# Kernel tuning notes

Measured on AMD Instinct MI355X. Metric: run time of the kernel, lower is better.

Reference implementation:

```python
import jax, jax.numpy as jnp
import numpy as np
from jax.ops import segment_sum, segment_max

N = 50000      # nodes
E_RAND = 800000
E = E_RAND + N  # random edges + self-loops
G = 4096       # graphs in batch
IN = 64        # input node feat dim
H = 4          # heads
F = 64         # per-head out feats
D = F          # gnn out feats (last agg = 'mean')
PH = 32        # predictor hidden (D // 2)
NEG_SLOPE = 0.2


def setup_inputs() -> dict:
    key = jax.random.key(0)
    ks = jax.random.split(key, 20)
    x = jax.random.normal(ks[0], (N, IN), dtype=jnp.float32)
    src = jnp.concatenate([jax.random.randint(ks[1], (E_RAND,), 0, N), jnp.arange(N)]).astype(jnp.int64)
    dst = jnp.concatenate([jax.random.randint(ks[2], (E_RAND,), 0, N), jnp.arange(N)]).astype(jnp.int64)
    gid = jnp.sort(jax.random.randint(ks[3], (N,), 0, G)).astype(jnp.int64)
    s = 0.1
    # layer 1: in=IN, flatten -> H*F
    W1 = jax.random.normal(ks[4], (IN, H * F), dtype=jnp.float32) * s
    al1 = jax.random.normal(ks[5], (H, F), dtype=jnp.float32) * s
    ar1 = jax.random.normal(ks[6], (H, F), dtype=jnp.float32) * s
    b1 = jnp.zeros((H * F,), dtype=jnp.float32)
    Wres1 = jax.random.normal(ks[7], (IN, H * F), dtype=jnp.float32) * s
    # layer 2: in=H*F, mean -> F
    W2 = jax.random.normal(ks[8], (H * F, H * F), dtype=jnp.float32) * s
    al2 = jax.random.normal(ks[9], (H, F), dtype=jnp.float32) * s
    ar2 = jax.random.normal(ks[10], (H, F), dtype=jnp.float32) * s
    b2 = jnp.zeros((H * F,), dtype=jnp.float32)
    Wres2 = jax.random.normal(ks[11], (H * F, H * F), dtype=jnp.float32) * s
    # WeightedSumAndMax atom-weighting
    Ww = jax.random.normal(ks[12], (D, 1), dtype=jnp.float32) * s
    bw = jnp.zeros((1,), dtype=jnp.float32)
    # predictor MLP: 2D -> PH -> 1
    Wp1 = jax.random.normal(ks[13], (2 * D, PH), dtype=jnp.float32) * s
    bp1 = jnp.zeros((PH,), dtype=jnp.float32)
    Wp2 = jax.random.normal(ks[14], (PH, 1), dtype=jnp.float32) * s
    bp2 = jnp.zeros((1,), dtype=jnp.float32)
    return dict(x=x, src=src, dst=dst, gid=gid,
                W1=W1, al1=al1, ar1=ar1, b1=b1, Wres1=Wres1,
                W2=W2, al2=al2, ar2=ar2, b2=b2, Wres2=Wres2,
                Ww=Ww, bw=bw, Wp1=Wp1, bp1=bp1, Wp2=Wp2, bp2=bp2)


def gat_conv(x, src, dst, W, al, ar, b, Wres, agg):
    n = x.shape[0]
    h, f = al.shape
    feat = (x @ W).reshape(n, h, f)                      # [N,H,F]
    el = jnp.einsum('nhf,hf->nh', feat, al)              # [N,H]
    er = jnp.einsum('nhf,hf->nh', feat, ar)
    e = jax.nn.leaky_relu(el[src] + er[dst], NEG_SLOPE)  # [E,H]
    # segment softmax over incoming edges per destination node
    m = segment_max(e, dst, num_segments=n)
    a = jnp.exp(e - m[dst])
    denom = segment_sum(a, dst, num_segments=n)
    attn = a / denom[dst]                                # [E,H]
    out = segment_sum(feat[src] * attn[:, :, None], dst, num_segments=n)  # [N,H,F]
    out = out + (x @ Wres).reshape(n, h, f) + b.reshape(1, h, f)
    out = jax.nn.elu(out)
    return out.reshape(n, h * f) if agg == 'flatten' else out.mean(axis=1)


def reference(x, src, dst, gid, W1, al1, ar1, b1, Wres1,
              W2, al2, ar2, b2, Wres2, Ww, bw, Wp1, bp1, Wp2, bp2):
    hfeat = gat_conv(x, src, dst, W1, al1, ar1, b1, Wres1, 'flatten')  # [N,H*F]
    hfeat = gat_conv(hfeat, src, dst, W2, al2, ar2, b2, Wres2, 'mean') # [N,F]
    # WeightedSumAndMax readout per graph
    w = jax.nn.sigmoid(hfeat @ Ww + bw)                                # [N,1]
    wsum = segment_sum(hfeat * w, gid, num_segments=G)                 # [G,F]
    hmax = segment_max(hfeat, gid, num_segments=G)                     # [G,F]
    gfeat = jnp.concatenate([wsum, hmax], axis=1)                      # [G,2F]
    return jax.nn.relu(gfeat @ Wp1 + bp1) @ Wp2 + bp2                  # [G,1]
```

## Files before the change

kernel.cpp:

```cpp
#include <hip/hip_runtime.h>
#include <hip/hip_bf16.h>
#include <math.h>

#define HF    256
#define HEADS 4
#define FD    64
#define NEG_SLOPE 0.2f

typedef __attribute__((ext_vector_type(8))) short short8;
typedef __attribute__((ext_vector_type(4))) float f32x4;

__device__ __forceinline__ float wave_sum(float v) {
  #pragma unroll
  for (int off = 32; off; off >>= 1) v += __shfl_xor(v, off);
  return v;
}

__device__ __forceinline__ unsigned short f2bf(float f) {
  unsigned u = __float_as_uint(f);
  u += 0x7FFFu + ((u >> 16) & 1u);
  return (unsigned short)(u >> 16);
}
__device__ __forceinline__ float bf2f(unsigned short u) {
  return __uint_as_float((unsigned)u << 16);
}

__device__ __forceinline__ void gload_lds16(const void* g, void* l) {
  __builtin_amdgcn_global_load_lds((const unsigned int*)g, (unsigned int*)l,
                                   16, 0, 0);
}

template<int K>
__global__ __launch_bounds__(256) void gemm_mfma(
    const unsigned short* __restrict__ A,
    const unsigned short* __restrict__ BT,
    const float* __restrict__ al, const float* __restrict__ ar,
    unsigned short* __restrict__ featbf, unsigned short* __restrict__ resbf,
    float* __restrict__ el, float* __restrict__ er, int M)
{
  __shared__ __align__(16) unsigned short As[128 * 32];
  __shared__ __align__(16) unsigned short Bs[128 * 32];
  const int t    = threadIdx.x;
  const int lane = t & 63, w = t >> 6;
  const int wr = w >> 1, wc = w & 1;
  const int l15 = lane & 15, lhi = lane >> 4;
  const int row0 = blockIdx.x * 128;
  const int n0b  = blockIdx.y;

  const int c0 = w * 128 + lane;
  const int c1 = c0 + 64;
  const unsigned short* gA0 = A  + (size_t)(row0 + (c0 >> 2)) * K + (c0 & 3) * 8;
  const unsigned short* gA1 = A  + (size_t)(row0 + (c1 >> 2)) * K + (c1 & 3) * 8;
  const unsigned short* gB0 = BT + (size_t)(n0b * 128 + (c0 >> 2)) * K + (c0 & 3) * 8;
  const unsigned short* gB1 = BT + (size_t)(n0b * 128 + (c1 >> 2)) * K + (c1 & 3) * 8;
  unsigned short* lA0 = &As[w * 1024];
  unsigned short* lA1 = &As[w * 1024 + 512];
  unsigned short* lB0 = &Bs[w * 1024];
  unsigned short* lB1 = &Bs[w * 1024 + 512];

  f32x4 acc[4][4];
  #pragma unroll
  for (int i = 0; i < 4; ++i)
    #pragma unroll
    for (int j = 0; j < 4; ++j)
      acc[i][j] = (f32x4){0.f, 0.f, 0.f, 0.f};

  for (int k0 = 0; k0 < K; k0 += 32) {
    __syncthreads();
    gload_lds16(gA0 + k0, lA0);
    gload_lds16(gA1 + k0, lA1);
    gload_lds16(gB0 + k0, lB0);
    gload_lds16(gB1 + k0, lB1);
    __syncthreads();

    short8 a[4], b[4];
    #pragma unroll
    for (int im = 0; im < 4; ++im)
      a[im] = *(const short8*)&As[(wr * 64 + im * 16 + l15) * 32 + lhi * 8];
    #pragma unroll
    for (int jn = 0; jn < 4; ++jn)
      b[jn] = *(const short8*)&Bs[(wc * 64 + jn * 16 + l15) * 32 + lhi * 8];
    #pragma unroll
    for (int im = 0; im < 4; ++im)
      #pragma unroll
      for (int jn = 0; jn < 4; ++jn)
        acc[im][jn] = __builtin_amdgcn_mfma_f32_16x16x32_bf16(
            a[im], b[jn], acc[im][jn], 0, 0, 0);
  }

  unsigned short* outp = (n0b < 2) ? featbf : resbf;
  const int colbase = (n0b & 1) * 128 + wc * 64;
  #pragma unroll
  for (int im = 0; im < 4; ++im) {
    const int rowb = row0 + wr * 64 + im * 16 + lhi * 4;
    #pragma unroll
    for (int q = 0; q < 4; ++q) {
      if (rowb + q < M) {
        unsigned short* rp = outp + (size_t)(rowb + q) * HF + colbase;
        #pragma unroll
        for (int jn = 0; jn < 4; ++jn)
          rp[jn * 16 + l15] = f2bf(acc[im][jn][q]);
      }
    }
  }

  if (n0b < 2) {
    const int hd = n0b * 2 + wc;
    float alv[4], arv[4];
    #pragma unroll
    for (int jn = 0; jn < 4; ++jn) {
      alv[jn] = al[hd * FD + jn * 16 + l15];
      arv[jn] = ar[hd * FD + jn * 16 + l15];
    }
    #pragma unroll
    for (int im = 0; im < 4; ++im) {
      #pragma unroll
      for (int q = 0; q < 4; ++q) {
        float es = 0.f, rs = 0.f;
        #pragma unroll
        for (int jn = 0; jn < 4; ++jn) {
          es = fmaf(acc[im][jn][q], alv[jn], es);
          rs = fmaf(acc[im][jn][q], arv[jn], rs);
        }
        #pragma unroll
        for (int off = 1; off < 16; off <<= 1) {
          es += __shfl_xor(es, off);
          rs += __shfl_xor(rs, off);
        }
        const int row = row0 + wr * 64 + im * 16 + lhi * 4 + q;
        if (l15 == 0 && row < M) {
          el[row * HEADS + hd] = es;
          er[row * HEADS + hd] = rs;
        }
      }
    }
  }
}

__global__ void k_cvt_init(
    const float* __restrict__ x,
    const float* __restrict__ W1, const float* __restrict__ Wres1,
    const float* __restrict__ W2, const float* __restrict__ Wres2,
    unsigned short* __restrict__ xbf, unsigned short* __restrict__ BT1,
    unsigned short* __restrict__ BT2, int* __restrict__ counts,
    int* __restrict__ cursor, float* __restrict__ wsum,
    unsigned* __restrict__ hmax, int n4, int N, int GFD)
{
  int i = blockIdx.x * 256 + threadIdx.x;
  if (i < n4) {
    float4 v = ((const float4*)x)[i];
    ushort4 o;
    o.x = f2bf(v.x); o.y = f2bf(v.y); o.z = f2bf(v.z); o.w = f2bf(v.w);
    ((ushort4*)xbf)[i] = o;
    return;
  }
  i -= n4;
  if (i < 512 * 64) {
    int j = i >> 6, k = i & 63;
    float v = (j < HF) ? W1[k * HF + j] : Wres1[k * HF + (j - HF)];
    BT1[i] = f2bf(v);
    return;
  }
  i -= 512 * 64;
  if (i < 512 * 256) {
    int j = i >> 8, k = i & 255;
    float v = (j < HF) ? W2[k * HF + j] : Wres2[k * HF + (j - HF)];
    BT2[i] = f2bf(v);
    return;
  }
  i -= 512 * 256;
  if (i < N) { counts[i] = 0; return; }
  i -= N;
  if (i < N) { cursor[i] = 0; return; }
  i -= N;
  if (i < GFD) { wsum[i] = 0.f; return; }
  i -= GFD;
  if (i < GFD) hmax[i] = 0x007FFFFFu;
}

__global__ void k_hist(const int* __restrict__ dst, int* __restrict__ counts, int E) {
  int i = blockIdx.x * 256 + threadIdx.x;
  if (i < E) atomicAdd(&counts[dst[i]], 1);
}

__global__ __launch_bounds__(256) void k_scan1(
    const int* __restrict__ counts, int* __restrict__ offs,
    int* __restrict__ bsum, int n)
{
  __shared__ int lds[256];
  const int b = blockIdx.x, t = threadIdx.x;
  const int base = b * 1024 + t * 4;
  int v[4];
  #pragma unroll
  for (int i = 0; i < 4; ++i) { int idx = base + i; v[i] = (idx < n) ? counts[idx] : 0; }
  int tsum = v[0] + v[1] + v[2] + v[3];
  lds[t] = tsum;
  __syncthreads();
  for (int off = 1; off < 256; off <<= 1) {
    int x = (t >= off) ? lds[t - off] : 0;
    __syncthreads();
    lds[t] += x;
    __syncthreads();
  }
  int run = lds[t] - tsum;
  #pragma unroll
  for (int i = 0; i < 4; ++i) {
    int idx = base + i;
    if (idx < n) offs[idx] = run;
    run += v[i];
  }
  if (t == 255) bsum[b] = lds[255];
}

__global__ void k_scan2(int* __restrict__ bsum, int nb, int* __restrict__ offs, int n) {
  const int t = threadIdx.x;
  if (nb <= 64) {
    int v = (t < nb) ? bsum[t] : 0;
    int inc = v;
    #pragma unroll
    for (int off = 1; off < 64; off <<= 1) {
      int u = __shfl_up(inc, off);
      if (t >= off) inc += u;
    }
    if (t < nb) bsum[t] = inc - v;
    int total = __shfl(inc, 63);
    if (t == 0) offs[n] = total;
  } else if (t == 0) {
    int run = 0;
    for (int b = 0; b < nb; ++b) { int x = bsum[b]; bsum[b] = run; run += x; }
    offs[n] = run;
  }
}

__global__ void k_scan3(int* __restrict__ offs, const int* __restrict__ bsum, int n) {
  int i = blockIdx.x * 256 + threadIdx.x;
  if (i < n) offs[i] += bsum[i >> 10];
}

__global__ void k_scatter(const int* __restrict__ src, const int* __restrict__ dst,
                          const int* __restrict__ offs, int* __restrict__ cursor,
                          int* __restrict__ csr_src, int E) {
  int i = blockIdx.x * 256 + threadIdx.x;
  if (i < E) {
    int d = dst[i];
    int pos = offs[d] + atomicAdd(&cursor[d], 1);
    csr_src[pos] = src[i];
  }
}

#define DCAP 128
__global__ __launch_bounds__(256) void agg_l1(
    const unsigned short* __restrict__ feat, const unsigned short* __restrict__ res,
    const float* __restrict__ el, const float* __restrict__ er,
    const float* __restrict__ bias, const int* __restrict__ csr_src,
    const int* __restrict__ offs, unsigned short* __restrict__ outbf)
{
  __shared__ int    ssrc[DCAP];
  __shared__ float  sw4[DCAP * 4];
  __shared__ float  sden[4][4];
  __shared__ float4 sacc[4][64];
  const int n = blockIdx.x;
  const int t = threadIdx.x;
  const int lane = t & 63, w = t >> 6;
  const int h = t & 3, j0 = t >> 2;
  const int hd = lane >> 4;
  const int s0  = offs[n];
  const int deg = offs[n + 1] - s0;
  const bool cached = (deg <= DCAP);

  if (cached) {
    const float ernh = er[n * HEADS + h];
    float dp = 0.f;
    for (int j = j0; j < deg; j += 64) {
      int s = csr_src[s0 + j];
      float sc = el[s * HEADS + h] + ernh;
      sc = sc > 0.f ? sc : NEG_SLOPE * sc;
      float wv = __expf(sc);
      sw4[j * 4 + h] = wv;
      if (h == 0) ssrc[j] = s;
      dp += wv;
    }
    #pragma unroll
    for (int off = 4; off < 64; off <<= 1) dp += __shfl_xor(dp, off);
    if (lane < 4) sden[w][lane] = dp;
  }
  __syncthreads();

  float4 acc = make_float4(0.f, 0.f, 0.f, 0.f);
  if (cached) {
    int j = w;
    for (; j + 4 < deg; j += 8) {
      int   sa = ssrc[j],         sb = ssrc[j + 4];
      float wa = sw4[j * 4 + hd], wb = sw4[(j + 4) * 4 + hd];
      ushort4 fa = *((const ushort4*)&feat[(size_t)sa * HF] + lane);
      ushort4 fb = *((const ushort4*)&feat[(size_t)sb * HF] + lane);
      acc.x = fmaf(wa, bf2f(fa.x), acc.x); acc.x = fmaf(wb, bf2f(fb.x), acc.x);
      acc.y = fmaf(wa, bf2f(fa.y), acc.y); acc.y = fmaf(wb, bf2f(fb.y), acc.y);
      acc.z = fmaf(wa, bf2f(fa.z), acc.z); acc.z = fmaf(wb, bf2f(fb.z), acc.z);
      acc.w = fmaf(wa, bf2f(fa.w), acc.w); acc.w = fmaf(wb, bf2f(fb.w), acc.w);
    }
    if (j < deg) {
      int   sa = ssrc[j];
      float wa = sw4[j * 4 + hd];
      ushort4 fa = *((const ushort4*)&feat[(size_t)sa * HF] + lane);
      acc.x = fmaf(wa, bf2f(fa.x), acc.x);
      acc.y = fmaf(wa, bf2f(fa.y), acc.y);
      acc.z = fmaf(wa, bf2f(fa.z), acc.z);
      acc.w = fmaf(wa, bf2f(fa.w), acc.w);
    }
  } else {
    const float ernd = er[n * HEADS + hd];
    float dpu = 0.f;
    for (int j = w; j < deg; j += 4) {
      int s = csr_src[s0 + j];
      float sc = el[s * HEADS + hd] + ernd;
      sc = sc > 0.f ? sc : NEG_SLOPE * sc;
      float wv = __expf(sc);
      dpu += wv;
      ushort4 fa = *((const ushort4*)&feat[(size_t)s * HF] + lane);
      acc.x = fmaf(wv, bf2f(fa.x), acc.x);
      acc.y = fmaf(wv, bf2f(fa.y), acc.y);
      acc.z = fmaf(wv, bf2f(fa.z), acc.z);
      acc.w = fmaf(wv, bf2f(fa.w), acc.w);
    }
    if ((lane & 15) == 0) sden[w][hd] = dpu;
  }
  sacc[w][lane] = acc;
  __syncthreads();

  if (w == 0) {
    float4 a0 = sacc[0][lane], a1 = sacc[1][lane],
           a2 = sacc[2][lane], a3 = sacc[3][lane];
    float denom = sden[0][hd] + sden[1][hd] + sden[2][hd] + sden[3][hd];
    float rden = 1.f / denom;
    ushort4 rv = *((const ushort4*)&res[(size_t)n * HF] + lane);
    float4  bv = *((const float4*)bias + lane);
    float v0 = (a0.x + a1.x + a2.x + a3.x) * rden + bf2f(rv.x) + bv.x;
    float v1 = (a0.y + a1.y + a2.y + a3.y) * rden + bf2f(rv.y) + bv.y;
    float v2 = (a0.z + a1.z + a2.z + a3.z) * rden + bf2f(rv.z) + bv.z;
    float v3 = (a0.w + a1.w + a2.w + a3.w) * rden + bf2f(rv.w) + bv.w;
    v0 = v0 > 0.f ? v0 : expm1f(v0);
    v1 = v1 > 0.f ? v1 : expm1f(v1);
    v2 = v2 > 0.f ? v2 : expm1f(v2);
    v3 = v3 > 0.f ? v3 : expm1f(v3);
    ushort4 o;
    o.x = f2bf(v0); o.y = f2bf(v1); o.z = f2bf(v2); o.w = f2bf(v3);
    *((ushort4*)&outbf[(size_t)n * HF] + lane) = o;
  }
}

__global__ __launch_bounds__(256) void agg_l2(
    const unsigned short* __restrict__ feat, const unsigned short* __restrict__ res,
    const float* __restrict__ el, const float* __restrict__ er,
    const float* __restrict__ bias, const int* __restrict__ csr_src,
    const int* __restrict__ offs, const int* __restrict__ gid,
    const float* __restrict__ Ww, const float* __restrict__ bw,
    float* __restrict__ wsum, unsigned* __restrict__ hmax)
{
  __shared__ int    ssrc[DCAP];
  __shared__ float  sw4[DCAP * 4];
  __shared__ float  sden[4][4];
  __shared__ float4 sacc[4][64];
  const int n = blockIdx.x;
  const int t = threadIdx.x;
  const int lane = t & 63, w = t >> 6;
  const int h = t & 3, j0 = t >> 2;
  const int hd = lane >> 4;
  const int s0  = offs[n];
  const int deg = offs[n + 1] - s0;
  const bool cached = (deg <= DCAP);

  if (cached) {
    const float ernh = er[n * HEADS + h];
    float dp = 0.f;
    for (int j = j0; j < deg; j += 64) {
      int s = csr_src[s0 + j];
      float sc = el[s * HEADS + h] + ernh;
      sc = sc > 0.f ? sc : NEG_SLOPE * sc;
      float wv = __expf(sc);
      sw4[j * 4 + h] = wv;
      if (h == 0) ssrc[j] = s;
      dp += wv;
    }
    #pragma unroll
    for (int off = 4; off < 64; off <<= 1) dp += __shfl_xor(dp, off);
    if (lane < 4) sden[w][lane] = dp;
  }
  __syncthreads();

  float4 acc = make_float4(0.f, 0.f, 0.f, 0.f);
  if (cached) {
    int j = w;
    for (; j + 4 < deg; j += 8) {
      int   sa = ssrc[j],         sb = ssrc[j + 4];
      float wa = sw4[j * 4 + hd], wb = sw4[(j + 4) * 4 + hd];
      ushort4 fa = *((const ushort4*)&feat[(size_t)sa * HF] + lane);
      ushort4 fb = *((const ushort4*)&feat[(size_t)sb * HF] + lane);
      acc.x = fmaf(wa, bf2f(fa.x), acc.x); acc.x = fmaf(wb, bf2f(fb.x), acc.x);
      acc.y = fmaf(wa, bf2f(fa.y), acc.y); acc.y = fmaf(wb, bf2f(fb.y), acc.y);
      acc.z = fmaf(wa, bf2f(fa.z), acc.z); acc.z = fmaf(wb, bf2f(fb.z), acc.z);
      acc.w = fmaf(wa, bf2f(fa.w), acc.w); acc.w = fmaf(wb, bf2f(fb.w), acc.w);
    }
    if (j < deg) {
      int   sa = ssrc[j];
      float wa = sw4[j * 4 + hd];
      ushort4 fa = *((const ushort4*)&feat[(size_t)sa * HF] + lane);
      acc.x = fmaf(wa, bf2f(fa.x), acc.x);
      acc.y = fmaf(wa, bf2f(fa.y), acc.y);
      acc.z = fmaf(wa, bf2f(fa.z), acc.z);
      acc.w = fmaf(wa, bf2f(fa.w), acc.w);
    }
  } else {
    const float ernd = er[n * HEADS + hd];
    float dpu = 0.f;
    for (int j = w; j < deg; j += 4) {
      int s = csr_src[s0 + j];
      float sc = el[s * HEADS + hd] + ernd;
      sc = sc > 0.f ? sc : NEG_SLOPE * sc;
      float wv = __expf(sc);
      dpu += wv;
      ushort4 fa = *((const ushort4*)&feat[(size_t)s * HF] + lane);
      acc.x = fmaf(wv, bf2f(fa.x), acc.x);
      acc.y = fmaf(wv, bf2f(fa.y), acc.y);
      acc.z = fmaf(wv, bf2f(fa.z), acc.z);
      acc.w = fmaf(wv, bf2f(fa.w), acc.w);
    }
    if ((lane & 15) == 0) sden[w][hd] = dpu;
  }
  sacc[w][lane] = acc;
  __syncthreads();

  if (w == 0) {
    float4 a0 = sacc[0][lane], a1 = sacc[1][lane],
           a2 = sacc[2][lane], a3 = sacc[3][lane];
    float denom = sden[0][hd] + sden[1][hd] + sden[2][hd] + sden[3][hd];
    float rden = 1.f / denom;
    ushort4 rv = *((const ushort4*)&res[(size_t)n * HF] + lane);
    float4  bv = *((const float4*)bias + lane);
    float v0 = (a0.x + a1.x + a2.x + a3.x) * rden + bf2f(rv.x) + bv.x;
    float v1 = (a0.y + a1.y + a2.y + a3.y) * rden + bf2f(rv.y) + bv.y;
    float v2 = (a0.z + a1.z + a2.z + a3.z) * rden + bf2f(rv.z) + bv.z;
    float v3 = (a0.w + a1.w + a2.w + a3.w) * rden + bf2f(rv.w) + bv.w;
    v0 = v0 > 0.f ? v0 : expm1f(v0);
    v1 = v1 > 0.f ? v1 : expm1f(v1);
    v2 = v2 > 0.f ? v2 : expm1f(v2);
    v3 = v3 > 0.f ? v3 : expm1f(v3);
    #pragma unroll
    for (int off = 16; off < 64; off <<= 1) {
      v0 += __shfl_xor(v0, off);
      v1 += __shfl_xor(v1, off);
      v2 += __shfl_xor(v2, off);
      v3 += __shfl_xor(v3, off);
    }
    if (lane < 16) {
      const float h0 = 0.25f * v0, h1 = 0.25f * v1,
                  h2 = 0.25f * v2, h3 = 0.25f * v3;
      const float4 wwv = ((const float4*)Ww)[lane];
      float part = h0 * wwv.x + h1 * wwv.y + h2 * wwv.z + h3 * wwv.w;
      #pragma unroll
      for (int off = 1; off < 16; off <<= 1)
        part += __shfl_xor(part, off);
      const float wgt = 1.f / (1.f + __expf(-(part + bw[0])));
      const int g = gid[n];
      float* wp = &wsum[g * FD + lane * 4];
      atomicAdd(wp + 0, h0 * wgt);
      atomicAdd(wp + 1, h1 * wgt);
      atomicAdd(wp + 2, h2 * wgt);
      atomicAdd(wp + 3, h3 * wgt);
      unsigned* hp = &hmax[g * FD + lane * 4];
      unsigned u0 = __float_as_uint(h0), u1 = __float_as_uint(h1),
               u2 = __float_as_uint(h2), u3 = __float_as_uint(h3);
      atomicMax(hp + 0, (u0 & 0x80000000u) ? ~u0 : (u0 | 0x80000000u));
      atomicMax(hp + 1, (u1 & 0x80000000u) ? ~u1 : (u1 | 0x80000000u));
      atomicMax(hp + 2, (u2 & 0x80000000u) ? ~u2 : (u2 | 0x80000000u));
      atomicMax(hp + 3, (u3 & 0x80000000u) ? ~u3 : (u3 | 0x80000000u));
    }
  }
}

__global__ __launch_bounds__(64) void k_predict(
    const float* __restrict__ wsum, const unsigned* __restrict__ hmax,
    const float* __restrict__ Wp1, const float* __restrict__ bp1,
    const float* __restrict__ Wp2, const float* __restrict__ bp2,
    float* __restrict__ out)
{
  const int g = blockIdx.x, t = threadIdx.x;
  float acc = 0.f;
  if (t < 32) {
    acc = bp1[t];
    #pragma unroll 4
    for (int k = 0; k < FD; ++k)
      acc = fmaf(wsum[g * FD + k], Wp1[k * 32 + t], acc);
    #pragma unroll 4
    for (int k = 0; k < FD; ++k) {
      unsigned e = hmax[g * FD + k];
      float hv = (e & 0x80000000u) ? __uint_as_float(e & 0x7FFFFFFFu)
                                   : __uint_as_float(~e);
      acc = fmaf(hv, Wp1[(FD + k) * 32 + t], acc);
    }
    acc = fmaxf(acc, 0.f) * Wp2[t];
  }
  acc = wave_sum(acc);
  if (t == 0) out[g] = acc + bp2[0];
}

extern "C" void kernel_launch(void* const* d_in, const int* in_sizes, int n_in,
                              void* d_out, int out_size, void* d_ws, size_t ws_size,
                              hipStream_t stream) {
  const float* x     = (const float*)d_in[0];
  const int*   src   = (const int*)  d_in[1];
  const int*   dst   = (const int*)  d_in[2];
  const int*   gid   = (const int*)  d_in[3];
  const float* W1    = (const float*)d_in[4];
  const float* al1   = (const float*)d_in[5];
  const float* ar1   = (const float*)d_in[6];
  const float* b1    = (const float*)d_in[7];
  const float* Wres1 = (const float*)d_in[8];
  const float* W2    = (const float*)d_in[9];
  const float* al2   = (const float*)d_in[10];
  const float* ar2   = (const float*)d_in[11];
  const float* b2    = (const float*)d_in[12];
  const float* Wres2 = (const float*)d_in[13];
  const float* Ww    = (const float*)d_in[14];
  const float* bw    = (const float*)d_in[15];
  const float* Wp1   = (const float*)d_in[16];
  const float* bp1   = (const float*)d_in[17];
  const float* Wp2   = (const float*)d_in[18];
  const float* bp2   = (const float*)d_in[19];
  float* out = (float*)d_out;

  const int N = in_sizes[3];
  const int E = in_sizes[1];
  const int G = out_size;
  const int Mpad = (N + 127) & ~127;
  const int GFD  = G * FD;

  char* p = (char*)d_ws;
  auto alloc = [&](size_t bytes) {
    char* r = p;
    p += (bytes + 255) & ~(size_t)255;
    return r;
  };
  unsigned short* featbf  = (unsigned short*)alloc((size_t)Mpad * HF * 2);
  unsigned short* resbf   = (unsigned short*)alloc((size_t)Mpad * HF * 2);
  float*          el      = (float*)         alloc((size_t)N * HEADS * 4);
  float*          er      = (float*)         alloc((size_t)N * HEADS * 4);
  int*            counts  = (int*)           alloc((size_t)N * 4);
  int*            cursor  = (int*)           alloc((size_t)N * 4);
  int*            offs    = (int*)           alloc((size_t)(N + 1) * 4);
  const int nb            = (N + 1023) / 1024;
  int*            bsum    = (int*)           alloc((size_t)nb * 4);
  int*            csr_src = (int*)           alloc((size_t)E * 4);
  float*          wsum    = (float*)         alloc((size_t)GFD * 4);
  unsigned*       hmax    = (unsigned*)      alloc((size_t)GFD * 4);
  unsigned short* xbf     = (unsigned short*)alloc((size_t)Mpad * 64 * 2);
  unsigned short* h1bf    = (unsigned short*)alloc((size_t)Mpad * HF * 2);
  unsigned short* BT1     = (unsigned short*)alloc((size_t)512 * 64 * 2);
  unsigned short* BT2     = (unsigned short*)alloc((size_t)512 * 256 * 2);
  (void)ws_size; (void)n_in;

  const int n4 = N * 64 / 4;
  const int init_total = n4 + 512 * 64 + 512 * 256 + N + N + GFD + GFD;
  k_cvt_init<<<(init_total + 255) / 256, 256, 0, stream>>>(
      x, W1, Wres1, W2, Wres2, xbf, BT1, BT2,
      counts, cursor, wsum, hmax, n4, N, GFD);

  k_hist   <<<(E + 255) / 256, 256, 0, stream>>>(dst, counts, E);
  k_scan1  <<<nb, 256, 0, stream>>>(counts, offs, bsum, N);
  k_scan2  <<<1, 64, 0, stream>>>(bsum, nb, offs, N);
  k_scan3  <<<(N + 255) / 256, 256, 0, stream>>>(offs, bsum, N);
  k_scatter<<<(E + 255) / 256, 256, 0, stream>>>(src, dst, offs, cursor, csr_src, E);

  dim3 gg(Mpad / 128, 4);

  gemm_mfma<64> <<<gg, 256, 0, stream>>>(xbf, BT1, al1, ar1,
                                         featbf, resbf, el, er, N);
  agg_l1        <<<N, 256, 0, stream>>>(featbf, resbf, el, er, b1, csr_src,
                                        offs, h1bf);

  gemm_mfma<256><<<gg, 256, 0, stream>>>(h1bf, BT2, al2, ar2,
                                         featbf, resbf, el, er, N);
  agg_l2        <<<N, 256, 0, stream>>>(featbf, resbf, el, er, b2, csr_src,
                                        offs, gid, Ww, bw, wsum, hmax);

  k_predict<<<G, 64, 0, stream>>>(wsum, hmax, Wp1, bp1, Wp2, bp2, out);
}
```

Before: 363.9 us.

## Replace atomic graph readout with sorted-gid segment offsets and fused reduce-predict kernel

Instead of per-node atomicAdd/atomicMax into per-graph accumulators, agg_l2 now writes each node's mean feature and sigmoid weight to global memory. Graph boundaries are computed from the sorted gid array in the init kernel, and a new kernel reduces each graph's node range per wave and then runs the predictor MLP. This removes contended float atomics and the zero/sentinel initialization, at the cost of an extra N×64 float write and read. It relies on gid being sorted.

```diff
diff --git a/kernel.cpp b/kernel.cpp
--- a/kernel.cpp
+++ b/kernel.cpp
@@ -143,8 +143,8 @@
     const float* __restrict__ W2, const float* __restrict__ Wres2,
     unsigned short* __restrict__ xbf, unsigned short* __restrict__ BT1,
     unsigned short* __restrict__ BT2, int* __restrict__ counts,
-    int* __restrict__ cursor, float* __restrict__ wsum,
-    unsigned* __restrict__ hmax, int n4, int N, int GFD)
+    int* __restrict__ cursor, const int* __restrict__ gid,
+    int* __restrict__ goffs, int n4, int N, int G)
 {
   int i = blockIdx.x * 256 + threadIdx.x;
   if (i < n4) {
@@ -173,9 +173,18 @@
   i -= N;
   if (i < N) { cursor[i] = 0; return; }
   i -= N;
-  if (i < GFD) { wsum[i] = 0.f; return; }
-  i -= GFD;
-  if (i < GFD) hmax[i] = 0x007FFFFFu;
+  if (i < N) {
+    const int g1 = gid[i];
+    if (i == 0) {
+      for (int g = 0; g <= g1; ++g) goffs[g] = 0;
+    } else {
+      const int g0 = gid[i - 1];
+      for (int g = g0 + 1; g <= g1; ++g) goffs[g] = i;
+    }
+    if (i == N - 1) {
+      for (int g = g1 + 1; g <= G; ++g) goffs[g] = N;
+    }
+  }
 }
 
 __global__ void k_hist(const int* __restrict__ dst, int* __restrict__ counts, int E) {
@@ -353,9 +362,9 @@
     const unsigned short* __restrict__ feat, const unsigned short* __restrict__ res,
     const float* __restrict__ el, const float* __restrict__ er,
     const float* __restrict__ bias, const int* __restrict__ csr_src,
-    const int* __restrict__ offs, const int* __restrict__ gid,
-    const float* __restrict__ Ww, const float* __restrict__ bw,
-    float* __restrict__ wsum, unsigned* __restrict__ hmax)
+    const int* __restrict__ offs, const float* __restrict__ Ww,
+    const float* __restrict__ bw, float* __restrict__ h2out,
+    float* __restrict__ node_w)
 {
   __shared__ int    ssrc[DCAP];
   __shared__ float  sw4[DCAP * 4];
@@ -453,55 +462,61 @@
       v3 += __shfl_xor(v3, off);
     }
     if (lane < 16) {
-      const float h0 = 0.25f * v0, h1 = 0.25f * v1,
-                  h2 = 0.25f * v2, h3 = 0.25f * v3;
+      const float m0 = 0.25f * v0, m1 = 0.25f * v1,
+                  m2 = 0.25f * v2, m3 = 0.25f * v3;
+      *((float4*)&h2out[(size_t)n * FD] + lane) = make_float4(m0, m1, m2, m3);
       const float4 wwv = ((const float4*)Ww)[lane];
-      float part = h0 * wwv.x + h1 * wwv.y + h2 * wwv.z + h3 * wwv.w;
+      float part = m0 * wwv.x + m1 * wwv.y + m2 * wwv.z + m3 * wwv.w;
       #pragma unroll
       for (int off = 1; off < 16; off <<= 1)
         part += __shfl_xor(part, off);
-      const float wgt = 1.f / (1.f + __expf(-(part + bw[0])));
-      const int g = gid[n];
-      float* wp = &wsum[g * FD + lane * 4];
-      atomicAdd(wp + 0, h0 * wgt);
-      atomicAdd(wp + 1, h1 * wgt);
-      atomicAdd(wp + 2, h2 * wgt);
-      atomicAdd(wp + 3, h3 * wgt);
-      unsigned* hp = &hmax[g * FD + lane * 4];
-      unsigned u0 = __float_as_uint(h0), u1 = __float_as_uint(h1),
-               u2 = __float_as_uint(h2), u3 = __float_as_uint(h3);
-      atomicMax(hp + 0, (u0 & 0x80000000u) ? ~u0 : (u0 | 0x80000000u));
-      atomicMax(hp + 1, (u1 & 0x80000000u) ? ~u1 : (u1 | 0x80000000u));
-      atomicMax(hp + 2, (u2 & 0x80000000u) ? ~u2 : (u2 | 0x80000000u));
-      atomicMax(hp + 3, (u3 & 0x80000000u) ? ~u3 : (u3 | 0x80000000u));
-    }
-  }
-}
-
-__global__ __launch_bounds__(64) void k_predict(
-    const float* __restrict__ wsum, const unsigned* __restrict__ hmax,
+      if (lane == 0)
+        node_w[n] = 1.f / (1.f + __expf(-(part + bw[0])));
+    }
+  }
+}
+
+__global__ __launch_bounds__(256) void k_rp(
+    const float* __restrict__ h2, const float* __restrict__ node_w,
+    const int* __restrict__ goffs,
     const float* __restrict__ Wp1, const float* __restrict__ bp1,
     const float* __restrict__ Wp2, const float* __restrict__ bp2,
-    float* __restrict__ out)
+    float* __restrict__ out, int G)
 {
-  const int g = blockIdx.x, t = threadIdx.x;
+  __shared__ float lws[4][FD];
+  __shared__ float lmx[4][FD];
+  const int w = threadIdx.x >> 6, lane = threadIdx.x & 63;
+  const int g = blockIdx.x * 4 + w;
+
+  float ws = 0.f, mx = -INFINITY;
+  if (g < G) {
+    const int n0 = goffs[g], n1 = goffs[g + 1];
+    for (int n = n0; n < n1; ++n) {
+      float v  = h2[(size_t)n * FD + lane];
+      float wn = node_w[n];
+      ws = fmaf(wn, v, ws);
+      mx = fmaxf(mx, v);
+    }
+  }
+  lws[w][lane] = ws;
+  lmx[w][lane] = mx;
+  __syncthreads();
+
   float acc = 0.f;
-  if (t < 32) {
-    acc = bp1[t];
+  if (g < G && lane < 32) {
+    acc = bp1[lane];
     #pragma unroll 4
     for (int k = 0; k < FD; ++k)
-      acc = fmaf(wsum[g * FD + k], Wp1[k * 32 + t], acc);
+      acc = fmaf(lws[w][k], Wp1[k * 32 + lane], acc);
     #pragma unroll 4
-    for (int k = 0; k < FD; ++k) {
-      unsigned e = hmax[g * FD + k];
-      float hv = (e & 0x80000000u) ? __uint_as_float(e & 0x7FFFFFFFu)
-                                   : __uint_as_float(~e);
-      acc = fmaf(hv, Wp1[(FD + k) * 32 + t], acc);
-    }
-    acc = fmaxf(acc, 0.f) * Wp2[t];
-  }
-  acc = wave_sum(acc);
-  if (t == 0) out[g] = acc + bp2[0];
+    for (int k = 0; k < FD; ++k)
+      acc = fmaf(lmx[w][k], Wp1[(FD + k) * 32 + lane], acc);
+    acc = fmaxf(acc, 0.f) * Wp2[lane];
+  }
+  #pragma unroll
+  for (int off = 1; off < 32; off <<= 1)
+    acc += __shfl_xor(acc, off);
+  if (g < G && lane == 0) out[g] = acc + bp2[0];
 }
 
 extern "C" void kernel_launch(void* const* d_in, const int* in_sizes, int n_in,
@@ -533,7 +548,6 @@
   const int E = in_sizes[1];
   const int G = out_size;
   const int Mpad = (N + 127) & ~127;
-  const int GFD  = G * FD;
 
   char* p = (char*)d_ws;
   auto alloc = [&](size_t bytes) {
@@ -551,8 +565,9 @@
   const int nb            = (N + 1023) / 1024;
   int*            bsum    = (int*)           alloc((size_t)nb * 4);
   int*            csr_src = (int*)           alloc((size_t)E * 4);
-  float*          wsum    = (float*)         alloc((size_t)GFD * 4);
-  unsigned*       hmax    = (unsigned*)      alloc((size_t)GFD * 4);
+  float*          h2      = (float*)         alloc((size_t)N * FD * 4);
+  float*          node_w  = (float*)         alloc((size_t)N * 4);
+  int*            goffs   = (int*)           alloc((size_t)(G + 1) * 4);
   unsigned short* xbf     = (unsigned short*)alloc((size_t)Mpad * 64 * 2);
   unsigned short* h1bf    = (unsigned short*)alloc((size_t)Mpad * HF * 2);
   unsigned short* BT1     = (unsigned short*)alloc((size_t)512 * 64 * 2);
@@ -560,10 +575,10 @@
   (void)ws_size; (void)n_in;
 
   const int n4 = N * 64 / 4;
-  const int init_total = n4 + 512 * 64 + 512 * 256 + N + N + GFD + GFD;
+  const int init_total = n4 + 512 * 64 + 512 * 256 + N + N + N;
   k_cvt_init<<<(init_total + 255) / 256, 256, 0, stream>>>(
       x, W1, Wres1, W2, Wres2, xbf, BT1, BT2,
-      counts, cursor, wsum, hmax, n4, N, GFD);
+      counts, cursor, gid, goffs, n4, N, G);
 
   k_hist   <<<(E + 255) / 256, 256, 0, stream>>>(dst, counts, E);
   k_scan1  <<<nb, 256, 0, stream>>>(counts, offs, bsum, N);
@@ -581,7 +596,8 @@
   gemm_mfma<256><<<gg, 256, 0, stream>>>(h1bf, BT2, al2, ar2,
                                          featbf, resbf, el, er, N);
   agg_l2        <<<N, 256, 0, stream>>>(featbf, resbf, el, er, b2, csr_src,
-                                        offs, gid, Ww, bw, wsum, hmax);
-
-  k_predict<<<G, 64, 0, stream>>>(wsum, hmax, Wp1, bp1, Wp2, bp2, out);
-}
+                                        offs, Ww, bw, h2, node_w);
+
+  k_rp<<<(G + 3) / 4, 256, 0, stream>>>(h2, node_w, goffs,
+                                        Wp1, bp1, Wp2, bp2, out, G);
+}
```

New measurement: 337.3 us, median of 2. 7.3% less time.
